# Kernel tuning notes

Hardware: AMD Instinct MI355X
Metric: run time of the kernel (lower is better)

Reference implementation:

```python
import jax, jax.numpy as jnp
import numpy as np

B, N, MODEL_D = 2, 1024, 2048
KQ_D, V_D, H, I = 128, 128, 8, 4
ROPE_THETA = 10000.0


def _rope(x, theta):
    # x: [b, n, ..., d]; positions along axis 1, rotation over last dim d.
    d = x.shape[-1]
    n = x.shape[1]
    inv_freq = theta ** (-jnp.arange(0, d, 2, dtype=jnp.float32) / d)  # [d/2]
    ang = jnp.arange(n, dtype=jnp.float32)[:, None] * inv_freq          # [n, d/2]
    bshape = (1, n) + (1,) * (x.ndim - 3) + (d // 2,)
    cos = jnp.cos(ang).reshape(bshape).astype(x.dtype)
    sin = jnp.sin(ang).reshape(bshape).astype(x.dtype)
    x1, x2 = jnp.split(x, 2, axis=-1)
    return jnp.concatenate([x1 * cos - x2 * sin, x1 * sin + x2 * cos], axis=-1)


def setup_inputs() -> dict:
    key = jax.random.key(0)
    kx, kq, kk, kv, ko = jax.random.split(key, 5)
    s_in = 1.0 / np.sqrt(MODEL_D)
    s_out = 1.0 / np.sqrt(H * I * V_D)
    x = jax.random.normal(kx, (B, N, MODEL_D), jnp.float32)
    Wq = jax.random.normal(kq, (MODEL_D, H, I, KQ_D), jnp.float32) * s_in
    Wk = jax.random.normal(kk, (MODEL_D, H, KQ_D), jnp.float32) * s_in
    Wv = jax.random.normal(kv, (MODEL_D, H, V_D), jnp.float32) * s_in
    Wo = jax.random.normal(ko, (H, I, V_D, MODEL_D), jnp.float32) * s_out
    return {"x": x, "Wq": Wq, "Wk": Wk, "Wv": Wv, "Wo": Wo}


def reference(x, Wq, Wk, Wv, Wo):
    # GQA projections (per Ueajsum specs)
    q = jnp.einsum('bnd,dhik->bnhik', x, Wq)   # [B,N,H,I,K]
    k = jnp.einsum('bnd,dhc->bnhc', x, Wk)     # [B,N,H,K]
    v = jnp.einsum('bnd,dhv->bnhv', x, Wv)     # [B,N,H,V]
    # RoPE on q and k
    q = _rope(q, ROPE_THETA)
    k = _rope(k, ROPE_THETA)
    # Causal softmax attention, each kv head serves I query heads
    scale = 1.0 / np.sqrt(KQ_D)
    scores = jnp.einsum('bnhic,bmhc->bhinm', q, k) * scale  # [B,H,I,N,N]
    n = x.shape[1]
    causal = jnp.tril(jnp.ones((n, n), dtype=bool))
    scores = jnp.where(causal, scores, jnp.finfo(scores.dtype).min)
    p = jax.nn.softmax(scores, axis=-1)
    out = jnp.einsum('bhinm,bmhv->bnhiv', p, v)              # [B,N,H,I,V]
    return jnp.einsum('bnhiv,hivd->bnd', out, Wo)            # [B,N,D]
```

## Files before the change

### kernel.cpp

```cpp
#include <hip/hip_runtime.h>
#include <hip/hip_bf16.h>

typedef __bf16 bf16x8 __attribute__((ext_vector_type(8)));
typedef float floatx4 __attribute__((ext_vector_type(4)));

static __device__ __forceinline__ void async_cp16(const __bf16* g, __bf16* l) {
    typedef const __attribute__((address_space(1))) unsigned int gu32;
    typedef __attribute__((address_space(3))) unsigned int lu32;
    __builtin_amdgcn_global_load_lds((gu32*)g, (lu32*)l, 16, 0, 0);
}

static __device__ __forceinline__ void tile64_f32(
    const float* __restrict__ src, __bf16* __restrict__ dst,
    int R, int C, int r0, int c0, int tid, __bf16* t )
{
    {
        const int r = tid >> 2, cq = (tid & 3) * 16;
        const float* p = src + (size_t)(r0 + r) * C + c0 + cq;
        float4 f0 = *(const float4*)(p);
        float4 f1 = *(const float4*)(p + 4);
        float4 f2 = *(const float4*)(p + 8);
        float4 f3 = *(const float4*)(p + 12);
        __bf16 v[16] = {
            (__bf16)f0.x, (__bf16)f0.y, (__bf16)f0.z, (__bf16)f0.w,
            (__bf16)f1.x, (__bf16)f1.y, (__bf16)f1.z, (__bf16)f1.w,
            (__bf16)f2.x, (__bf16)f2.y, (__bf16)f2.z, (__bf16)f2.w,
            (__bf16)f3.x, (__bf16)f3.y, (__bf16)f3.z, (__bf16)f3.w };
        #pragma unroll
        for (int e = 0; e < 16; ++e) t[(cq + e) * 72 + r] = v[e];
    }
    __syncthreads();
    {
        const int c = tid >> 2, rq = (tid & 3) * 16;
        uint4 u0 = *(const uint4*)(&t[c * 72 + rq]);
        uint4 u1 = *(const uint4*)(&t[c * 72 + rq + 8]);
        __bf16* q = dst + (size_t)(c0 + c) * R + r0 + rq;
        *(uint4*)(q)     = u0;
        *(uint4*)(q + 8) = u1;
    }
}

static __device__ __forceinline__ void tile64_b16(
    const __bf16* __restrict__ src, __bf16* __restrict__ dst,
    int src_ld, int dst_ld, int tid, __bf16* t )
{
    {
        const int r = tid >> 2, cq = (tid & 3) * 16;
        const __bf16* p = src + (size_t)r * src_ld + cq;
        union { uint4 u; __bf16 b[8]; } a0, a1;
        a0.u = *(const uint4*)(p);
        a1.u = *(const uint4*)(p + 8);
        #pragma unroll
        for (int e = 0; e < 8; ++e) {
            t[(cq + e) * 72 + r]     = a0.b[e];
            t[(cq + 8 + e) * 72 + r] = a1.b[e];
        }
    }
    __syncthreads();
    {
        const int c = tid >> 2, rq = (tid & 3) * 16;
        uint4 u0 = *(const uint4*)(&t[c * 72 + rq]);
        uint4 u1 = *(const uint4*)(&t[c * 72 + rq + 8]);
        __bf16* q = dst + (size_t)c * dst_ld + rq;
        *(uint4*)(q)     = u0;
        *(uint4*)(q + 8) = u1;
    }
}

__global__ __launch_bounds__(256) void prep_kernel(
    const float* __restrict__ x,  __bf16* __restrict__ xb,
    const float* __restrict__ Wq, const float* __restrict__ Wk,
    const float* __restrict__ Wv, __bf16* __restrict__ Wt)
{
    __shared__ __bf16 t[64 * 72];
    const int bk  = blockIdx.x;
    const int tid = threadIdx.x;

    if (bk < 2048) {
        int ct = bk & 63, rt = bk >> 6;
        tile64_f32(Wq, Wt, 2048, 4096, rt * 64, ct * 64, tid, t);
    } else if (bk < 2560) {
        int idx = bk - 2048, ct = idx & 15, rt = idx >> 4;
        tile64_f32(Wk, Wt + (size_t)4096 * 2048, 2048, 1024, rt * 64, ct * 64, tid, t);
    } else if (bk < 3072) {
        int idx = bk - 2560, ct = idx & 15, rt = idx >> 4;
        tile64_f32(Wv, Wt + (size_t)5120 * 2048, 2048, 1024, rt * 64, ct * 64, tid, t);
    } else {
        int idx = (bk - 3072) * 256 + tid;
        const float* p = x + (size_t)idx * 8;
        float4 f0 = *(const float4*)p;
        float4 f1 = *(const float4*)(p + 4);
        union { uint4 u; __bf16 b[8]; } o;
        o.b[0] = (__bf16)f0.x; o.b[1] = (__bf16)f0.y; o.b[2] = (__bf16)f0.z; o.b[3] = (__bf16)f0.w;
        o.b[4] = (__bf16)f1.x; o.b[5] = (__bf16)f1.y; o.b[6] = (__bf16)f1.z; o.b[7] = (__bf16)f1.w;
        *(uint4*)(xb + (size_t)idx * 8) = o.u;
    }
}

__global__ __launch_bounds__(256) void rope_vtrans_wot_kernel(
    __bf16* __restrict__ qkv, __bf16* __restrict__ vt,
    const float* __restrict__ Wo, __bf16* __restrict__ WoT)
{
    __shared__ __bf16 t[64 * 72];
    const int bk  = blockIdx.x;
    const int tid = threadIdx.x;

    if (bk < 2560) {
        int idx  = bk * 256 + tid;
        int part = idx & 7;
        int tt   = idx >> 3;
        int head = tt % 40;
        int row  = tt / 40;
        int n    = row & 1023;
        int col0 = (head < 32) ? head * 128 : 4096 + (head - 32) * 128;
        size_t base = (size_t)row * 6144 + col0 + part * 8;

        union { uint4 u; __bf16 b[8]; } x1, x2, o1, o2;
        x1.u = *(const uint4*)(qkv + base);
        x2.u = *(const uint4*)(qkv + base + 64);
        #pragma unroll
        for (int e = 0; e < 8; ++e) {
            int j = part * 8 + e;
            float inv_freq = exp2f(-(float)j * 0.20762050593046015f);
            float ang = (float)n * inv_freq;
            float sv, cv;
            __sincosf(ang, &sv, &cv);
            float a = (float)x1.b[e], b2 = (float)x2.b[e];
            o1.b[e] = (__bf16)(a * cv - b2 * sv);
            o2.b[e] = (__bf16)(a * sv + b2 * cv);
        }
        *(uint4*)(qkv + base)      = o1.u;
        *(uint4*)(qkv + base + 64) = o2.u;
    } else if (bk < 3072) {
        int idx = bk - 2560;
        int bh = idx >> 5, rem = idx & 31;
        int k0 = (rem >> 1) * 64, v0 = (rem & 1) * 64;
        int b = bh >> 3, h = bh & 7;
        const __bf16* src = qkv + (size_t)(b * 1024 + k0) * 6144 + 5120 + h * 128 + v0;
        __bf16* dst = vt + ((size_t)bh * 128 + v0) * 1024 + k0;
        tile64_b16(src, dst, 6144, 1024, tid, t);
    } else {
        int idx = bk - 3072;
        int ct = idx & 31, rt = idx >> 5;
        tile64_f32(Wo, WoT, 4096, 2048, rt * 64, ct * 64, tid, t);
    }
}

__global__ __launch_bounds__(256) void gemm_bt(
    const __bf16* __restrict__ A,
    const __bf16* __restrict__ Bt,
    __bf16* __restrict__ C,
    int M, int lda, int ldb, int ldc,
    int kc_base, int kc_extra)
{
    __shared__ __bf16 As[128 * 64];
    __shared__ __bf16 Bs[128 * 64];

    const int tid  = threadIdx.x;
    const int wave = tid >> 6;
    const int lane = tid & 63;
    const int quad = lane >> 4;
    const int l15  = lane & 15;
    const int wr   = wave >> 1, wc = wave & 1;

    const int bm = blockIdx.y * 128;
    const int bn = blockIdx.x * 128;
    const int z  = blockIdx.z;
    const int Kc = kc_base + ((z == (int)gridDim.z - 1) ? kc_extra : 0);

    A  += (size_t)z * kc_base;
    Bt += (size_t)z * kc_base;
    C  += (size_t)z * M * ldc;

    floatx4 acc[16];
    #pragma unroll
    for (int i = 0; i < 16; ++i) acc[i] = floatx4{0.f, 0.f, 0.f, 0.f};

    const int sr = lane >> 3;
    const int sc = ((lane & 7) ^ sr) * 8;
    const __bf16* a0 = A  + (size_t)(bm + wave * 32 + sr) * lda + sc;
    const __bf16* b0 = Bt + (size_t)(bn + wave * 32 + sr) * ldb + sc;
    __bf16* asd = As + (wave * 32) * 64;
    __bf16* bsd = Bs + (wave * 32) * 64;

    for (int k0 = 0; k0 < Kc; k0 += 64) {
        __syncthreads();
        #pragma unroll
        for (int r = 0; r < 4; ++r) {
            async_cp16(a0 + (size_t)(r * 8) * lda + k0, asd + (r * 8) * 64);
            async_cp16(b0 + (size_t)(r * 8) * ldb + k0, bsd + (r * 8) * 64);
        }
        __syncthreads();

        #pragma unroll
        for (int ko = 0; ko < 2; ++ko) {
            bf16x8 af[4], bf[4];
            #pragma unroll
            for (int t = 0; t < 4; ++t)
                af[t] = *(const bf16x8*)(
                    &As[(wr * 64 + t * 16 + l15) * 64 + (((ko * 4 + quad) ^ (l15 & 7)) * 8)]);
            #pragma unroll
            for (int u = 0; u < 4; ++u)
                bf[u] = *(const bf16x8*)(
                    &Bs[(wc * 64 + u * 16 + l15) * 64 + (((ko * 4 + quad) ^ (l15 & 7)) * 8)]);
            #pragma unroll
            for (int t = 0; t < 4; ++t)
                #pragma unroll
                for (int u = 0; u < 4; ++u)
                    acc[t * 4 + u] = __builtin_amdgcn_mfma_f32_16x16x32_bf16(
                        af[t], bf[u], acc[t * 4 + u], 0, 0, 0);
        }
    }

    #pragma unroll
    for (int t = 0; t < 4; ++t)
        #pragma unroll
        for (int u = 0; u < 4; ++u)
            #pragma unroll
            for (int r = 0; r < 4; ++r) {
                int row = bm + wr * 64 + t * 16 + quad * 4 + r;
                int col = bn + wc * 64 + u * 16 + l15;
                C[(size_t)row * ldc + col] = (__bf16)acc[t * 4 + u][r];
            }
}

__global__ __launch_bounds__(256) void reduce_kernel(
    const __bf16* __restrict__ part, float* __restrict__ out)
{
    int idx = blockIdx.x * 256 + threadIdx.x;
    const size_t S = (size_t)2048 * 2048;
    union { uint4 u; __bf16 b[8]; } p0, p1, p2;
    p0.u = *(const uint4*)(part + (size_t)idx * 8);
    p1.u = *(const uint4*)(part + S + (size_t)idx * 8);
    p2.u = *(const uint4*)(part + 2 * S + (size_t)idx * 8);
    float4 o0, o1;
    o0.x = (float)p0.b[0] + (float)p1.b[0] + (float)p2.b[0];
    o0.y = (float)p0.b[1] + (float)p1.b[1] + (float)p2.b[1];
    o0.z = (float)p0.b[2] + (float)p1.b[2] + (float)p2.b[2];
    o0.w = (float)p0.b[3] + (float)p1.b[3] + (float)p2.b[3];
    o1.x = (float)p0.b[4] + (float)p1.b[4] + (float)p2.b[4];
    o1.y = (float)p0.b[5] + (float)p1.b[5] + (float)p2.b[5];
    o1.z = (float)p0.b[6] + (float)p1.b[6] + (float)p2.b[6];
    o1.w = (float)p0.b[7] + (float)p1.b[7] + (float)p2.b[7];
    *(float4*)(out + (size_t)idx * 8)     = o0;
    *(float4*)(out + (size_t)idx * 8 + 4) = o1;
}

__global__ __launch_bounds__(512, 2) void attn_kernel(
    const __bf16* __restrict__ qkv,
    const __bf16* __restrict__ vt,
    __bf16* __restrict__ ao)
{
    const int PS_LD = 72;
    __shared__ __bf16 Ks[64 * 128];
    __shared__ __bf16 Vs[128 * 64];
    __shared__ __bf16 Ps[8][16 * PS_LD];

    const int tid  = threadIdx.x;
    const int wave = tid >> 6;
    const int lane = tid & 63;
    const int quad = lane >> 4;
    const int l15  = lane & 15;
    const int i    = wave >> 1;
    const int rt   = wave & 1;

    const int pair = blockIdx.x;
    const int bh   = blockIdx.y;
    const int b    = bh >> 3, h = bh & 7;
    const __bf16* vtb = vt + (size_t)bh * 128 * 1024;

    const int keyA = wave * 8 + (lane >> 4);
    const int keyB = keyA + 4;
    const int chA  = (lane & 15) ^ (keyA & 15);
    const int chB  = (lane & 15) ^ (keyB & 15);
    const __bf16* gK0 = qkv + (size_t)(b * 1024 + keyA) * 6144 + 4096 + h * 128 + chA * 8;
    const __bf16* gK1 = qkv + (size_t)(b * 1024 + keyB) * 6144 + 4096 + h * 128 + chB * 8;
    __bf16* lK0 = Ks + (wave * 8) * 128;
    __bf16* lK1 = Ks + (wave * 8 + 4) * 128;

    const int vdA = wave * 16 + (lane >> 3);
    const int vdB = vdA + 8;
    const int cvA = (lane & 7) ^ (vdA & 7);
    const int cvB = (lane & 7) ^ (vdB & 7);
    const __bf16* gV0 = vtb + (size_t)vdA * 1024 + cvA * 8;
    const __bf16* gV1 = vtb + (size_t)vdB * 1024 + cvB * 8;
    __bf16* lV0 = Vs + (wave * 16) * 64;
    __bf16* lV1 = Vs + (wave * 16 + 8) * 64;

    bf16x8 onesf;
    #pragma unroll
    for (int j = 0; j < 8; ++j) onesf[j] = (__bf16)1.0f;

    const float C2 = 0.12751898549f;

    #pragma unroll
    for (int ph = 0; ph < 2; ++ph) {
        const int qt    = ph ? (31 - pair) : pair;
        const int qrow0 = qt * 32 + rt * 16;

        const __bf16* qp = qkv + (size_t)(b * 1024 + qrow0 + l15) * 6144 + (h * 4 + i) * 128;
        bf16x8 qf[4];
        #pragma unroll
        for (int c = 0; c < 4; ++c)
            qf[c] = *(const bf16x8*)(qp + c * 32 + quad * 8);

        floatx4 acc[8];
        #pragma unroll
        for (int u = 0; u < 8; ++u) acc[u] = floatx4{0.f, 0.f, 0.f, 0.f};
        floatx4 accl = floatx4{0.f, 0.f, 0.f, 0.f};

        const int ntiles = (qt >> 1) + 1;

        uint4 rk0 = *(const uint4*)(gK0);
        uint4 rk1 = *(const uint4*)(gK1);
        uint4 rv0 = *(const uint4*)(gV0);
        uint4 rv1 = *(const uint4*)(gV1);

        for (int t = 0; t < ntiles; ++t) {
            const int kt = t * 64;
            __syncthreads();
            *(uint4*)(lK0 + lane * 8) = rk0;
            *(uint4*)(lK1 + lane * 8) = rk1;
            *(uint4*)(lV0 + lane * 8) = rv0;
            *(uint4*)(lV1 + lane * 8) = rv1;
            if (t + 1 < ntiles) {
                const int kt1 = kt + 64;
                rk0 = *(const uint4*)(gK0 + (size_t)kt1 * 6144);
                rk1 = *(const uint4*)(gK1 + (size_t)kt1 * 6144);
                rv0 = *(const uint4*)(gV0 + kt1);
                rv1 = *(const uint4*)(gV1 + kt1);
            }
            __syncthreads();

            floatx4 s[4];
            #pragma unroll
            for (int ks = 0; ks < 4; ++ks) s[ks] = floatx4{0.f, 0.f, 0.f, 0.f};
            #pragma unroll
            for (int c = 0; c < 4; ++c) {
                #pragma unroll
                for (int ks = 0; ks < 4; ++ks) {
                    bf16x8 kf = *(const bf16x8*)(
                        &Ks[(ks * 16 + l15) * 128 + ((c * 4 + quad) ^ l15) * 8]);
                    s[ks] = __builtin_amdgcn_mfma_f32_16x16x32_bf16(qf[c], kf, s[ks], 0, 0, 0);
                }
            }

            #pragma unroll
            for (int r = 0; r < 4; ++r) {
                int qrow = qrow0 + quad * 4 + r;
                #pragma unroll
                for (int ks = 0; ks < 4; ++ks) {
                    int kc = kt + ks * 16 + l15;
                    float p = (kc <= qrow) ? exp2f(s[ks][r] * C2) : 0.0f;
                    Ps[wave][(quad * 4 + r) * PS_LD + ks * 16 + l15] = (__bf16)p;
                }
            }

            #pragma unroll
            for (int s2 = 0; s2 < 2; ++s2) {
                bf16x8 pa = *(const bf16x8*)(&Ps[wave][l15 * PS_LD + s2 * 32 + quad * 8]);
                accl = __builtin_amdgcn_mfma_f32_16x16x32_bf16(pa, onesf, accl, 0, 0, 0);
                #pragma unroll
                for (int u = 0; u < 8; ++u) {
                    bf16x8 vf = *(const bf16x8*)(
                        &Vs[(u * 16 + l15) * 64 + (((s2 * 4 + quad) ^ (l15 & 7))) * 8]);
                    acc[u] = __builtin_amdgcn_mfma_f32_16x16x32_bf16(pa, vf, acc[u], 0, 0, 0);
                }
            }
        }

        #pragma unroll
        for (int r = 0; r < 4; ++r) {
            float inv = 1.0f / accl[r];
            int row = qrow0 + quad * 4 + r;
            __bf16* op = ao + (size_t)(b * 1024 + row) * 4096 + (h * 4 + i) * 128;
            #pragma unroll
            for (int u = 0; u < 8; ++u)
                op[u * 16 + l15] = (__bf16)(acc[u][r] * inv);
        }
    }
}

extern "C" void kernel_launch(void* const* d_in, const int* in_sizes, int n_in,
                              void* d_out, int out_size, void* d_ws, size_t ws_size,
                              hipStream_t stream)
{
    const float* x  = (const float*)d_in[0];
    const float* Wq = (const float*)d_in[1];
    const float* Wk = (const float*)d_in[2];
    const float* Wv = (const float*)d_in[3];
    const float* Wo = (const float*)d_in[4];
    float* out = (float*)d_out;

    const size_t MB = 1024 * 1024;
    char* ws = (char*)d_ws;
    __bf16* qkv  = (__bf16*)(ws);
    __bf16* vtb  = (__bf16*)(ws + 24 * MB);
    __bf16* xb   = (__bf16*)(ws + 28 * MB);
    __bf16* Wt   = (__bf16*)(ws + 36 * MB);
    __bf16* WoT  = (__bf16*)(ws + 28 * MB);
    __bf16* ao   = (__bf16*)(ws + 44 * MB);
    __bf16* part = (__bf16*)(ws);

    prep_kernel<<<5120, 256, 0, stream>>>(x, xb, Wq, Wk, Wv, Wt);
    gemm_bt<<<dim3(48, 16), 256, 0, stream>>>(xb, Wt, qkv, 2048, 2048, 2048, 6144, 2048, 0);
    rope_vtrans_wot_kernel<<<5120, 256, 0, stream>>>(qkv, vtb, Wo, WoT);
    attn_kernel<<<dim3(16, 16), 512, 0, stream>>>(qkv, vtb, ao);
    gemm_bt<<<dim3(16, 16, 3), 256, 0, stream>>>(ao, WoT, part, 2048, 4096, 4096, 2048, 1344, 64);
    reduce_kernel<<<2048, 256, 0, stream>>>(part, out);
}
```

Baseline: 282.7 us.

## Give each attention wave two 16-row query tiles, halving block size

After: 291.2 us. 3.0% more time.

```diff
diff --git a/kernel.cpp b/kernel.cpp
--- a/kernel.cpp
+++ b/kernel.cpp
@@ -246,7 +246,7 @@
     *(float4*)(out + (size_t)idx * 8 + 4) = o1;
 }
 
-__global__ __launch_bounds__(512, 2) void attn_kernel(
+__global__ __launch_bounds__(256) void attn_kernel(
     const __bf16* __restrict__ qkv,
     const __bf16* __restrict__ vt,
     __bf16* __restrict__ ao)
@@ -254,38 +254,49 @@
     const int PS_LD = 72;
     __shared__ __bf16 Ks[64 * 128];
     __shared__ __bf16 Vs[128 * 64];
-    __shared__ __bf16 Ps[8][16 * PS_LD];
+    __shared__ __bf16 Ps[4][32 * PS_LD];
 
     const int tid  = threadIdx.x;
     const int wave = tid >> 6;
     const int lane = tid & 63;
     const int quad = lane >> 4;
     const int l15  = lane & 15;
-    const int i    = wave >> 1;
-    const int rt   = wave & 1;
+    const int i    = wave;
 
     const int pair = blockIdx.x;
     const int bh   = blockIdx.y;
     const int b    = bh >> 3, h = bh & 7;
     const __bf16* vtb = vt + (size_t)bh * 128 * 1024;
 
-    const int keyA = wave * 8 + (lane >> 4);
-    const int keyB = keyA + 4;
+    const int keyA = wave * 16 + (lane >> 4);
+    const int keyB = keyA + 4, keyC = keyA + 8, keyD = keyA + 12;
     const int chA  = (lane & 15) ^ (keyA & 15);
     const int chB  = (lane & 15) ^ (keyB & 15);
+    const int chC  = (lane & 15) ^ (keyC & 15);
+    const int chD  = (lane & 15) ^ (keyD & 15);
     const __bf16* gK0 = qkv + (size_t)(b * 1024 + keyA) * 6144 + 4096 + h * 128 + chA * 8;
     const __bf16* gK1 = qkv + (size_t)(b * 1024 + keyB) * 6144 + 4096 + h * 128 + chB * 8;
-    __bf16* lK0 = Ks + (wave * 8) * 128;
-    __bf16* lK1 = Ks + (wave * 8 + 4) * 128;
-
-    const int vdA = wave * 16 + (lane >> 3);
-    const int vdB = vdA + 8;
+    const __bf16* gK2 = qkv + (size_t)(b * 1024 + keyC) * 6144 + 4096 + h * 128 + chC * 8;
+    const __bf16* gK3 = qkv + (size_t)(b * 1024 + keyD) * 6144 + 4096 + h * 128 + chD * 8;
+    __bf16* lK0 = Ks + (wave * 16) * 128;
+    __bf16* lK1 = Ks + (wave * 16 + 4) * 128;
+    __bf16* lK2 = Ks + (wave * 16 + 8) * 128;
+    __bf16* lK3 = Ks + (wave * 16 + 12) * 128;
+
+    const int vdA = wave * 32 + (lane >> 3);
+    const int vdB = vdA + 8, vdC = vdA + 16, vdD = vdA + 24;
     const int cvA = (lane & 7) ^ (vdA & 7);
     const int cvB = (lane & 7) ^ (vdB & 7);
+    const int cvC = (lane & 7) ^ (vdC & 7);
+    const int cvD = (lane & 7) ^ (vdD & 7);
     const __bf16* gV0 = vtb + (size_t)vdA * 1024 + cvA * 8;
     const __bf16* gV1 = vtb + (size_t)vdB * 1024 + cvB * 8;
-    __bf16* lV0 = Vs + (wave * 16) * 64;
-    __bf16* lV1 = Vs + (wave * 16 + 8) * 64;
+    const __bf16* gV2 = vtb + (size_t)vdC * 1024 + cvC * 8;
+    const __bf16* gV3 = vtb + (size_t)vdD * 1024 + cvD * 8;
+    __bf16* lV0 = Vs + (wave * 32) * 64;
+    __bf16* lV1 = Vs + (wave * 32 + 8) * 64;
+    __bf16* lV2 = Vs + (wave * 32 + 16) * 64;
+    __bf16* lV3 = Vs + (wave * 32 + 24) * 64;
 
     bf16x8 onesf;
     #pragma unroll
@@ -296,88 +307,126 @@
     #pragma unroll
     for (int ph = 0; ph < 2; ++ph) {
         const int qt    = ph ? (31 - pair) : pair;
-        const int qrow0 = qt * 32 + rt * 16;
-
-        const __bf16* qp = qkv + (size_t)(b * 1024 + qrow0 + l15) * 6144 + (h * 4 + i) * 128;
-        bf16x8 qf[4];
-        #pragma unroll
-        for (int c = 0; c < 4; ++c)
-            qf[c] = *(const bf16x8*)(qp + c * 32 + quad * 8);
-
-        floatx4 acc[8];
-        #pragma unroll
-        for (int u = 0; u < 8; ++u) acc[u] = floatx4{0.f, 0.f, 0.f, 0.f};
-        floatx4 accl = floatx4{0.f, 0.f, 0.f, 0.f};
+        const int qrow0 = qt * 32;
+
+        bf16x8 qf[2][4];
+        #pragma unroll
+        for (int m = 0; m < 2; ++m) {
+            const __bf16* qp = qkv + (size_t)(b * 1024 + qrow0 + m * 16 + l15) * 6144
+                             + (h * 4 + i) * 128;
+            #pragma unroll
+            for (int c = 0; c < 4; ++c)
+                qf[m][c] = *(const bf16x8*)(qp + c * 32 + quad * 8);
+        }
+
+        floatx4 acc[2][8];
+        #pragma unroll
+        for (int m = 0; m < 2; ++m)
+            #pragma unroll
+            for (int u = 0; u < 8; ++u) acc[m][u] = floatx4{0.f, 0.f, 0.f, 0.f};
+        floatx4 accl[2];
+        accl[0] = floatx4{0.f, 0.f, 0.f, 0.f};
+        accl[1] = floatx4{0.f, 0.f, 0.f, 0.f};
 
         const int ntiles = (qt >> 1) + 1;
 
         uint4 rk0 = *(const uint4*)(gK0);
         uint4 rk1 = *(const uint4*)(gK1);
+        uint4 rk2 = *(const uint4*)(gK2);
+        uint4 rk3 = *(const uint4*)(gK3);
         uint4 rv0 = *(const uint4*)(gV0);
         uint4 rv1 = *(const uint4*)(gV1);
+        uint4 rv2 = *(const uint4*)(gV2);
+        uint4 rv3 = *(const uint4*)(gV3);
 
         for (int t = 0; t < ntiles; ++t) {
             const int kt = t * 64;
             __syncthreads();
             *(uint4*)(lK0 + lane * 8) = rk0;
             *(uint4*)(lK1 + lane * 8) = rk1;
+            *(uint4*)(lK2 + lane * 8) = rk2;
+            *(uint4*)(lK3 + lane * 8) = rk3;
             *(uint4*)(lV0 + lane * 8) = rv0;
             *(uint4*)(lV1 + lane * 8) = rv1;
+            *(uint4*)(lV2 + lane * 8) = rv2;
+            *(uint4*)(lV3 + lane * 8) = rv3;
             if (t + 1 < ntiles) {
                 const int kt1 = kt + 64;
                 rk0 = *(const uint4*)(gK0 + (size_t)kt1 * 6144);
                 rk1 = *(const uint4*)(gK1 + (size_t)kt1 * 6144);
+                rk2 = *(const uint4*)(gK2 + (size_t)kt1 * 6144);
+                rk3 = *(const uint4*)(gK3 + (size_t)kt1 * 6144);
                 rv0 = *(const uint4*)(gV0 + kt1);
                 rv1 = *(const uint4*)(gV1 + kt1);
+                rv2 = *(const uint4*)(gV2 + kt1);
+                rv3 = *(const uint4*)(gV3 + kt1);
             }
             __syncthreads();
 
-            floatx4 s[4];
-            #pragma unroll
-            for (int ks = 0; ks < 4; ++ks) s[ks] = floatx4{0.f, 0.f, 0.f, 0.f};
+            floatx4 s[2][4];
+            #pragma unroll
+            for (int m = 0; m < 2; ++m)
+                #pragma unroll
+                for (int ks = 0; ks < 4; ++ks) s[m][ks] = floatx4{0.f, 0.f, 0.f, 0.f};
             #pragma unroll
             for (int c = 0; c < 4; ++c) {
                 #pragma unroll
                 for (int ks = 0; ks < 4; ++ks) {
                     bf16x8 kf = *(const bf16x8*)(
                         &Ks[(ks * 16 + l15) * 128 + ((c * 4 + quad) ^ l15) * 8]);
-                    s[ks] = __builtin_amdgcn_mfma_f32_16x16x32_bf16(qf[c], kf, s[ks], 0, 0, 0);
+                    #pragma unroll
+                    for (int m = 0; m < 2; ++m)
+                        s[m][ks] = __builtin_amdgcn_mfma_f32_16x16x32_bf16(
+                            qf[m][c], kf, s[m][ks], 0, 0, 0);
                 }
             }
 
             #pragma unroll
-            for (int r = 0; r < 4; ++r) {
-                int qrow = qrow0 + quad * 4 + r;
-                #pragma unroll
-                for (int ks = 0; ks < 4; ++ks) {
-                    int kc = kt + ks * 16 + l15;
-                    float p = (kc <= qrow) ? exp2f(s[ks][r] * C2) : 0.0f;
-                    Ps[wave][(quad * 4 + r) * PS_LD + ks * 16 + l15] = (__bf16)p;
+            for (int m = 0; m < 2; ++m)
+                #pragma unroll
+                for (int r = 0; r < 4; ++r) {
+                    int qrow = qrow0 + m * 16 + quad * 4 + r;
+                    #pragma unroll
+                    for (int ks = 0; ks < 4; ++ks) {
+                        int kc = kt + ks * 16 + l15;
+                        float p = (kc <= qrow) ? exp2f(s[m][ks][r] * C2) : 0.0f;
+                        Ps[wave][(m * 16 + quad * 4 + r) * PS_LD + ks * 16 + l15] = (__bf16)p;
+                    }
                 }
-            }
 
             #pragma unroll
             for (int s2 = 0; s2 < 2; ++s2) {
-                bf16x8 pa = *(const bf16x8*)(&Ps[wave][l15 * PS_LD + s2 * 32 + quad * 8]);
-                accl = __builtin_amdgcn_mfma_f32_16x16x32_bf16(pa, onesf, accl, 0, 0, 0);
+                bf16x8 pa[2];
+                #pragma unroll
+                for (int m = 0; m < 2; ++m) {
+                    pa[m] = *(const bf16x8*)(
+                        &Ps[wave][(m * 16 + l15) * PS_LD + s2 * 32 + quad * 8]);
+                    accl[m] = __builtin_amdgcn_mfma_f32_16x16x32_bf16(
+                        pa[m], onesf, accl[m], 0, 0, 0);
+                }
                 #pragma unroll
                 for (int u = 0; u < 8; ++u) {
                     bf16x8 vf = *(const bf16x8*)(
                         &Vs[(u * 16 + l15) * 64 + (((s2 * 4 + quad) ^ (l15 & 7))) * 8]);
-                    acc[u] = __builtin_amdgcn_mfma_f32_16x16x32_bf16(pa, vf, acc[u], 0, 0, 0);
+                    #pragma unroll
+                    for (int m = 0; m < 2; ++m)
+                        acc[m][u] = __builtin_amdgcn_mfma_f32_16x16x32_bf16(
+                            pa[m], vf, acc[m][u], 0, 0, 0);
                 }
             }
         }
 
         #pragma unroll
-        for (int r = 0; r < 4; ++r) {
-            float inv = 1.0f / accl[r];
-            int row = qrow0 + quad * 4 + r;
-            __bf16* op = ao + (size_t)(b * 1024 + row) * 4096 + (h * 4 + i) * 128;
-            #pragma unroll
-            for (int u = 0; u < 8; ++u)
-                op[u * 16 + l15] = (__bf16)(acc[u][r] * inv);
-        }
+        for (int m = 0; m < 2; ++m)
+            #pragma unroll
+            for (int r = 0; r < 4; ++r) {
+                float inv = 1.0f / accl[m][r];
+                int row = qrow0 + m * 16 + quad * 4 + r;
+                __bf16* op = ao + (size_t)(b * 1024 + row) * 4096 + (h * 4 + i) * 128;
+                #pragma unroll
+                for (int u = 0; u < 8; ++u)
+                    op[u * 16 + l15] = (__bf16)(acc[m][u][r] * inv);
+            }
     }
 }
 
@@ -405,7 +454,7 @@
     prep_kernel<<<5120, 256, 0, stream>>>(x, xb, Wq, Wk, Wv, Wt);
     gemm_bt<<<dim3(48, 16), 256, 0, stream>>>(xb, Wt, qkv, 2048, 2048, 2048, 6144, 2048, 0);
     rope_vtrans_wot_kernel<<<5120, 256, 0, stream>>>(qkv, vtb, Wo, WoT);
-    attn_kernel<<<dim3(16, 16), 512, 0, stream>>>(qkv, vtb, ao);
+    attn_kernel<<<dim3(16, 16), 256, 0, stream>>>(qkv, vtb, ao);
     gemm_bt<<<dim3(16, 16, 3), 256, 0, stream>>>(ao, WoT, part, 2048, 4096, 4096, 2048, 1344, 64);
     reduce_kernel<<<2048, 256, 0, stream>>>(part, out);
 }
```
